# Optimization experiments

Measured on AMD Instinct MI355X. Metric: run time of the kernel, lower is better.

## Reference

```python
import jax, jax.numpy as jnp
from jax import lax
import numpy as np
import math

B, H, W = 2, 48, 48
D_MODEL, D_STATE, D_CONV, EXPAND = 96, 16, 3, 2
D_INNER = EXPAND * D_MODEL
DT_RANK = math.ceil(D_MODEL / 16)
K = 6
L = H * W


def setup_inputs():
    key = jax.random.key(0)
    ks = jax.random.split(key, 10)
    x = jax.random.normal(ks[0], (B, H, W, D_MODEL), jnp.float32)
    y = jax.random.normal(ks[1], (B, H, W, D_MODEL), jnp.float32)
    k = jax.random.normal(ks[2], (B, H, W, D_MODEL), jnp.float32)
    in_proj_w = jax.random.normal(ks[3], (2 * D_INNER, D_MODEL), jnp.float32) * 0.02
    conv_w = jax.random.normal(ks[4], (D_INNER, 1, D_CONV, D_CONV), jnp.float32) * 0.1
    conv_b = jnp.zeros((D_INNER,), jnp.float32)
    x_proj_w = jax.random.normal(ks[5], (K, DT_RANK + 2 * D_STATE, D_INNER), jnp.float32) * 0.02
    s = DT_RANK ** -0.5
    dt_w = jax.random.uniform(ks[6], (K, D_INNER, DT_RANK), jnp.float32, -s, s)
    dt = jnp.exp(jax.random.uniform(ks[7], (K, D_INNER), jnp.float32)
                 * (math.log(0.1) - math.log(0.001)) + math.log(0.001))
    dt_b = dt + jnp.log(-jnp.expm1(-dt))  # inverse-softplus init as in dt_init
    A_logs = jnp.tile(jnp.log(jnp.arange(1, D_STATE + 1, dtype=jnp.float32))[None],
                      (K * D_INNER, 1))
    Ds = jnp.ones((K * D_INNER,), jnp.float32)
    ln_w = jnp.ones((D_INNER,), jnp.float32)
    ln_b = jnp.zeros((D_INNER,), jnp.float32)
    out_proj_w = jax.random.normal(ks[8], (D_MODEL, D_INNER), jnp.float32) * 0.02
    return dict(x=x, y=y, k=k, in_proj_w=in_proj_w, conv_w=conv_w, conv_b=conv_b,
                x_proj_w=x_proj_w, dt_w=dt_w, dt_b=dt_b, A_logs=A_logs, Ds=Ds,
                ln_w=ln_w, ln_b=ln_b, out_proj_w=out_proj_w)


def _diag_gather(t):
    # out[b,c,h,w] = t[b,c,h,(h+w)%W]; then (H,W)->(W,H) transpose, flatten
    idx = (jnp.arange(H)[:, None] + jnp.arange(W)[None, :]) % W
    g = jnp.take_along_axis(t, idx[None, None], axis=3)
    return jnp.swapaxes(g, -1, -2).reshape(t.shape[0], t.shape[1], L)


def _diag_scatter(flat):
    # inverse of _diag_gather: result[b,c,h,w] = r[b,c,h,(w-h)%W]
    r = jnp.swapaxes(flat.reshape(flat.shape[0], flat.shape[1], W, H), -1, -2)
    inv = (jnp.arange(W)[None, :] - jnp.arange(H)[:, None]) % W
    return jnp.take_along_axis(r, inv[None, None], axis=3)


def _forward(x, y, k, in_proj_w, conv_w, conv_b, x_proj_w, dt_w, dt_b,
             A_logs, Ds, ln_w, ln_b, out_proj_w):
    xv = jnp.einsum('bhwc,oc->bhwo', x, in_proj_w)[..., :D_INNER]
    yv = jnp.einsum('bhwc,oc->bhwo', y, in_proj_w)[..., :D_INNER]
    # NOTE: torch code overwrites z three times; the surviving gate z comes from k
    z = jnp.einsum('bhwc,oc->bhwo', k, in_proj_w)[..., D_INNER:]

    def conv_act(t):
        t = jnp.transpose(t, (0, 3, 1, 2))  # NCHW
        t = lax.conv_general_dilated(t, conv_w, (1, 1), ((1, 1), (1, 1)),
                                     feature_group_count=D_INNER,
                                     dimension_numbers=('NCHW', 'OIHW', 'NCHW'))
        return jax.nn.silu(t + conv_b[None, :, None, None])

    xc = conv_act(xv)  # (B,d,H,W)
    yc = conv_act(yv)

    h_x = xc.reshape(B, D_INNER, L)                                   # row-major
    v_y = jnp.swapaxes(yc, 2, 3).reshape(B, D_INNER, L)               # column-major
    diag_z = _diag_gather(yc)                                         # diagonal
    highfreq = jnp.stack([h_x, v_y, diag_z], axis=1)                  # (B,3,d,L)
    xs = jnp.concatenate([highfreq, jnp.flip(highfreq, axis=-1)], axis=1)  # (B,K,d,L)

    x_dbl = jnp.einsum('bkdl,kcd->bkcl', xs, x_proj_w)
    dts = jnp.einsum('bkrl,kdr->bkdl', x_dbl[:, :, :DT_RANK], dt_w)
    Bs = x_dbl[:, :, DT_RANK:DT_RANK + D_STATE]                       # (B,K,N,L)
    Cs = x_dbl[:, :, DT_RANK + D_STATE:]                              # (B,K,N,L)

    delta = jax.nn.softplus(dts + dt_b[None, :, :, None])             # (B,K,d,L)
    A = -jnp.exp(A_logs).reshape(K, D_INNER, D_STATE)
    Dk = Ds.reshape(K, D_INNER)

    def step(h, inp):
        dl, ul, Bl, Cl = inp  # (B,K,d),(B,K,d),(B,K,N),(B,K,N)
        h = jnp.exp(dl[..., None] * A) * h + (dl * ul)[..., None] * Bl[:, :, None, :]
        return h, jnp.einsum('bkdn,bkn->bkd', h, Cl)

    h0 = jnp.zeros((B, K, D_INNER, D_STATE), jnp.float32)
    seq = (jnp.moveaxis(delta, -1, 0), jnp.moveaxis(xs, -1, 0),
           jnp.moveaxis(Bs, -1, 0), jnp.moveaxis(Cs, -1, 0))
    _, ys = lax.scan(step, h0, seq)
    out_y = jnp.moveaxis(ys, 0, -1) + Dk[None, :, :, None] * xs       # (B,K,d,L)

    inv_y = jnp.flip(out_y[:, 3:6], axis=-1)

    def unT(t):  # undo the (W,H) raster used by vertical direction
        return jnp.swapaxes(t.reshape(B, D_INNER, W, H), -1, -2).reshape(B, D_INNER, L)

    y_h = out_y[:, 0] + inv_y[:, 0]
    y_v = unT(out_y[:, 1]) + unT(inv_y[:, 1])
    y_D = (_diag_scatter(out_y[:, 2]) + _diag_scatter(inv_y[:, 2])).reshape(B, D_INNER, L)

    zg = jax.nn.silu(z)

    def head(t):
        t = jnp.swapaxes(t, 1, 2).reshape(B, H, W, D_INNER)
        mu = t.mean(-1, keepdims=True)
        var = ((t - mu) ** 2).mean(-1, keepdims=True)
        t = (t - mu) * lax.rsqrt(var + 1e-5) * ln_w + ln_b
        return jnp.einsum('bhwd,od->bhwo', t * zg, out_proj_w)

    return head(y_h), head(y_v), head(y_D)


def reference(x, y, k, in_proj_w, conv_w, conv_b, x_proj_w, dt_w, dt_b,
              A_logs, Ds, ln_w, ln_b, out_proj_w):
    return _forward(x, y, k, in_proj_w, conv_w, conv_b, x_proj_w, dt_w, dt_b,
                    A_logs, Ds, ln_w, ln_b, out_proj_w)
```

## Files before the change

### kernel.cpp

```cpp
#include <hip/hip_runtime.h>
#include <hip/hip_bf16.h>

namespace {

constexpr int B_ = 2, H_ = 48, W_ = 48, DM_ = 96, DI_ = 192, NS_ = 16, RK_ = 6, K_ = 6;
constexpr int L_ = H_ * W_;
constexpr int C_ = 144;
constexpr int LC_ = L_ / C_;
constexpr int NPROJ = RK_ + 2 * NS_;
constexpr int NPAD = 48;

__device__ __forceinline__ float sigmoidf_(float x) { return 1.f / (1.f + __expf(-x)); }

__device__ __forceinline__ float delta_of(const float* __restrict__ dp,
                                          const float* __restrict__ wdt,
                                          float bias) {
  float s = bias;
#pragma unroll
  for (int r = 0; r < RK_; ++r) s += dp[r] * wdt[r];
  return (s > 20.f) ? s : __logf(1.f + __expf(s));
}

__device__ __forceinline__ int src_row(int k, int pos) {
  int pk = (k >= 3) ? (L_ - 1 - pos) : pos;
  int kk = (k >= 3) ? k - 3 : k;
  if (kk == 0) return pk;
  int h = pk % H_, wcol = pk / H_;
  if (kk == 1) return h * W_ + wcol;
  return h * W_ + (wcol + h) % W_;
}

constexpr int IM = 32, IBK = 32;
__global__ void __launch_bounds__(256) k_inproj2(
    const float* __restrict__ x, const float* __restrict__ y,
    const float* __restrict__ kin, const float* __restrict__ inpw,
    float* __restrict__ xv, float* __restrict__ yv, float* __restrict__ zg) {
  __shared__ float As[IM][IBK + 1];
  __shared__ float Ws[IBK][DI_ + 1];
  int tid = threadIdx.x;
  constexpr int BPS = (B_ * L_) / IM;
  int s = blockIdx.x / BPS;
  int row0 = (blockIdx.x % BPS) * IM;
  const float* src = (s == 0) ? x : (s == 1) ? y : kin;
  float* dst = (s == 0) ? xv : (s == 1) ? yv : zg;
  int nbase = (s == 2) ? DI_ : 0;
  int tm = tid >> 4, tn = tid & 15;
  float acc[2][12];
#pragma unroll
  for (int i = 0; i < 2; ++i)
#pragma unroll
    for (int j = 0; j < 12; ++j) acc[i][j] = 0.f;

  for (int k0 = 0; k0 < DM_; k0 += IBK) {
    {
      int r = tid >> 3, c4 = (tid & 7) << 2;
      const float4 v = *reinterpret_cast<const float4*>(
          &src[(size_t)(row0 + r) * DM_ + k0 + c4]);
      As[r][c4] = v.x; As[r][c4 + 1] = v.y; As[r][c4 + 2] = v.z; As[r][c4 + 3] = v.w;
    }
#pragma unroll
    for (int it = 0; it < 6; ++it) {
      int i = tid + it * 256;
      int col = i >> 3, k4 = (i & 7) << 2;
      const float4 v = *reinterpret_cast<const float4*>(
          &inpw[(size_t)(nbase + col) * DM_ + k0 + k4]);
      Ws[k4 + 0][col] = v.x; Ws[k4 + 1][col] = v.y;
      Ws[k4 + 2][col] = v.z; Ws[k4 + 3][col] = v.w;
    }
    __syncthreads();
#pragma unroll
    for (int kk = 0; kk < IBK; ++kk) {
      float a0 = As[tm * 2 + 0][kk], a1 = As[tm * 2 + 1][kk];
      float w[12];
#pragma unroll
      for (int j = 0; j < 12; ++j) w[j] = Ws[kk][tn * 12 + j];
#pragma unroll
      for (int j = 0; j < 12; ++j) {
        acc[0][j] += a0 * w[j];
        acc[1][j] += a1 * w[j];
      }
    }
    __syncthreads();
  }
#pragma unroll
  for (int i = 0; i < 2; ++i) {
    size_t ob = (size_t)(row0 + tm * 2 + i) * DI_ + tn * 12;
#pragma unroll
    for (int j4 = 0; j4 < 3; ++j4) {
      float4 v;
      v.x = acc[i][j4 * 4 + 0]; v.y = acc[i][j4 * 4 + 1];
      v.z = acc[i][j4 * 4 + 2]; v.w = acc[i][j4 * 4 + 3];
      if (s == 2) {
        v.x *= sigmoidf_(v.x); v.y *= sigmoidf_(v.y);
        v.z *= sigmoidf_(v.z); v.w *= sigmoidf_(v.w);
      }
      *reinterpret_cast<float4*>(&dst[ob + j4 * 4]) = v;
    }
  }
}

__global__ void __launch_bounds__(192) k_conv2(
    const float* __restrict__ xv, const float* __restrict__ yv,
    const float* __restrict__ cw, const float* __restrict__ cb,
    float* __restrict__ xc, float* __restrict__ yc) {
  __shared__ float scw[9 * DI_];
  int tid = threadIdx.x;
  for (int i = tid; i < 9 * DI_; i += 192) {
    int d = i / 9, j = i % 9;
    scw[j * DI_ + d] = cw[i];
  }
  __syncthreads();
  int p = tid / 48, q = tid % 48;
  int gl = blockIdx.x * 4 + p;
  int b = gl / L_, l = gl % L_;
  int h = l / W_, w = l % W_;
  int d4 = q << 2;
  float4 ax = *reinterpret_cast<const float4*>(&cb[d4]);
  float4 ay = ax;
#pragma unroll
  for (int kh = 0; kh < 3; ++kh) {
    int hh = h + kh - 1;
    if ((unsigned)hh >= (unsigned)H_) continue;
#pragma unroll
    for (int kw = 0; kw < 3; ++kw) {
      int ww = w + kw - 1;
      if ((unsigned)ww >= (unsigned)W_) continue;
      float4 wk = *reinterpret_cast<const float4*>(&scw[(kh * 3 + kw) * DI_ + d4]);
      size_t idx = ((size_t)b * L_ + hh * W_ + ww) * DI_ + d4;
      float4 vx = *reinterpret_cast<const float4*>(&xv[idx]);
      float4 vy = *reinterpret_cast<const float4*>(&yv[idx]);
      ax.x += vx.x * wk.x; ax.y += vx.y * wk.y; ax.z += vx.z * wk.z; ax.w += vx.w * wk.w;
      ay.x += vy.x * wk.x; ay.y += vy.y * wk.y; ay.z += vy.z * wk.z; ay.w += vy.w * wk.w;
    }
  }
  ax.x *= sigmoidf_(ax.x); ax.y *= sigmoidf_(ax.y);
  ax.z *= sigmoidf_(ax.z); ax.w *= sigmoidf_(ax.w);
  ay.x *= sigmoidf_(ay.x); ay.y *= sigmoidf_(ay.y);
  ay.z *= sigmoidf_(ay.z); ay.w *= sigmoidf_(ay.w);
  size_t ob = (size_t)gl * DI_ + d4;
  *reinterpret_cast<float4*>(&xc[ob]) = ax;
  *reinterpret_cast<float4*>(&yc[ob]) = ay;
}

constexpr int XM = 32, XBK = 32;
__global__ void __launch_bounds__(256) k_xdbl3(
    const float* __restrict__ xc, const float* __restrict__ yc,
    const float* __restrict__ xpw,
    float* __restrict__ dts, float* __restrict__ Bsb, float* __restrict__ Csb) {
  __shared__ float As[XM][XBK + 1];
  __shared__ float Ws[XBK][NPAD];
  int tid = threadIdx.x;
  int row0 = blockIdx.x * XM;
  int b = row0 / (K_ * L_);
  int k = (row0 / L_) % K_;
  int pos0 = row0 % L_;
  const float* usrc = ((k == 0 || k == 3) ? xc : yc) + (size_t)b * L_ * DI_;
  int tm = tid >> 4, tn = tid & 15;
  for (int i = tid; i < XBK * (NPAD - NPROJ); i += 256) {
    int kk = i / (NPAD - NPROJ), c = NPROJ + i % (NPAD - NPROJ);
    Ws[kk][c] = 0.f;
  }
  float acc[2][3];
#pragma unroll
  for (int i = 0; i < 2; ++i)
#pragma unroll
    for (int j = 0; j < 3; ++j) acc[i][j] = 0.f;

  for (int k0 = 0; k0 < DI_; k0 += XBK) {
    {
      int r = tid >> 3, c4 = (tid & 7) << 2;
      int srow = src_row(k, pos0 + r);
      const float4 v = *reinterpret_cast<const float4*>(
          &usrc[(size_t)srow * DI_ + k0 + c4]);
      As[r][c4] = v.x; As[r][c4 + 1] = v.y; As[r][c4 + 2] = v.z; As[r][c4 + 3] = v.w;
    }
#pragma unroll
    for (int it = 0; it < 2; ++it) {
      int i = tid + it * 256;
      if (i < NPROJ * 8) {
        int c = i >> 3, k4 = (i & 7) << 2;
        const float4 v = *reinterpret_cast<const float4*>(
            &xpw[((size_t)k * NPROJ + c) * DI_ + k0 + k4]);
        Ws[k4 + 0][c] = v.x; Ws[k4 + 1][c] = v.y;
        Ws[k4 + 2][c] = v.z; Ws[k4 + 3][c] = v.w;
      }
    }
    __syncthreads();
#pragma unroll
    for (int kk = 0; kk < XBK; ++kk) {
      float a0 = As[tm * 2 + 0][kk], a1 = As[tm * 2 + 1][kk];
      float w0 = Ws[kk][tn * 3 + 0], w1 = Ws[kk][tn * 3 + 1], w2 = Ws[kk][tn * 3 + 2];
      acc[0][0] += a0 * w0; acc[0][1] += a0 * w1; acc[0][2] += a0 * w2;
      acc[1][0] += a1 * w0; acc[1][1] += a1 * w1; acc[1][2] += a1 * w2;
    }
    __syncthreads();
  }
#pragma unroll
  for (int i = 0; i < 2; ++i) {
    int row = row0 + tm * 2 + i;
#pragma unroll
    for (int j = 0; j < 3; ++j) {
      int cc = tn * 3 + j;
      float v = acc[i][j];
      if (cc < RK_) dts[(size_t)row * RK_ + cc] = v;
      else if (cc < RK_ + NS_) Bsb[(size_t)row * NS_ + (cc - RK_)] = v;
      else if (cc < NPROJ) Csb[(size_t)row * NS_ + (cc - RK_ - NS_)] = v;
    }
  }
}

__global__ void __launch_bounds__(192) k_scan1(
    const float* __restrict__ dts, const float* __restrict__ dtw,
    const float* __restrict__ dtb, const float* __restrict__ xc,
    const float* __restrict__ yc, const float* __restrict__ Bsb,
    const float* __restrict__ A_logs,
    float* __restrict__ Sdl, float* __restrict__ SHin) {
  __shared__ float sB[LC_ * NS_];
  __shared__ float sdt[LC_ * RK_];
  int blk = blockIdx.x;
  int bk = blk / C_, c = blk % C_;
  int b = bk / K_, k = bk % K_;
  int d = threadIdx.x;
  const float* usrc = ((k == 0 || k == 3) ? xc : yc) + (size_t)b * L_ * DI_;
  int pos0 = c * LC_;
  size_t base = (size_t)bk * L_ + pos0;
  for (int i = d; i < LC_ * NS_; i += 192) sB[i] = Bsb[base * NS_ + i];
  for (int i = d; i < LC_ * RK_; i += 192) sdt[i] = dts[base * RK_ + i];
  float A[NS_];
#pragma unroll
  for (int n = 0; n < NS_; ++n) A[n] = -__expf(A_logs[((size_t)k * DI_ + d) * NS_ + n]);
  float wdt[RK_];
#pragma unroll
  for (int r = 0; r < RK_; ++r) wdt[r] = dtw[((size_t)k * DI_ + d) * RK_ + r];
  float bias = dtb[k * DI_ + d];
  float S[NS_];
#pragma unroll
  for (int n = 0; n < NS_; ++n) S[n] = 0.f;
  float sum_dl = 0.f;
  __syncthreads();
  for (int l = 0; l < LC_; ++l) {
    float dl = delta_of(&sdt[l * RK_], wdt, bias);
    float u = usrc[(size_t)src_row(k, pos0 + l) * DI_ + d];
    float du = dl * u;
    sum_dl += dl;
    const float* Bp = &sB[l * NS_];
#pragma unroll
    for (int n = 0; n < NS_; ++n) {
      float e = __expf(dl * A[n]);
      S[n] = e * S[n] + du * Bp[n];
    }
  }
  Sdl[(size_t)blk * DI_ + d] = sum_dl;
  size_t ob = (size_t)blk * NS_ * DI_ + d;
#pragma unroll
  for (int n = 0; n < NS_; ++n) SHin[ob + (size_t)n * DI_] = S[n];
}

__global__ void __launch_bounds__(192) k_scan2(
    const float* __restrict__ Sdl, const float* __restrict__ A_logs,
    float* __restrict__ SHin) {
  int bkn = blockIdx.x;
  int bk = bkn / NS_, n = bkn % NS_;
  int k = bk % K_;
  int d = threadIdx.x;
  float A = -__expf(A_logs[((size_t)k * DI_ + d) * NS_ + n]);
  float h = 0.f;
  for (int c = 0; c < C_; ++c) {
    size_t i = ((size_t)(bk * C_ + c) * NS_ + n) * DI_ + d;
    float s = SHin[i];
    float p = __expf(A * Sdl[(size_t)(bk * C_ + c) * DI_ + d]);
    SHin[i] = h;
    h = p * h + s;
  }
}

__global__ void __launch_bounds__(192) k_scan3(
    const float* __restrict__ dts, const float* __restrict__ dtw,
    const float* __restrict__ dtb, const float* __restrict__ xc,
    const float* __restrict__ yc, const float* __restrict__ Bsb,
    const float* __restrict__ Csb, const float* __restrict__ A_logs,
    const float* __restrict__ Ds, const float* __restrict__ SHin,
    float* __restrict__ out_y) {
  __shared__ float sB[LC_ * NS_];
  __shared__ float sC[LC_ * NS_];
  __shared__ float sdt[LC_ * RK_];
  int blk = blockIdx.x;
  int bk = blk / C_, c = blk % C_;
  int b = bk / K_, k = bk % K_;
  int d = threadIdx.x;
  const float* usrc = ((k == 0 || k == 3) ? xc : yc) + (size_t)b * L_ * DI_;
  int pos0 = c * LC_;
  size_t base = (size_t)bk * L_ + pos0;
  for (int i = d; i < LC_ * NS_; i += 192) {
    sB[i] = Bsb[base * NS_ + i];
    sC[i] = Csb[base * NS_ + i];
  }
  for (int i = d; i < LC_ * RK_; i += 192) sdt[i] = dts[base * RK_ + i];
  float A[NS_];
#pragma unroll
  for (int n = 0; n < NS_; ++n) A[n] = -__expf(A_logs[((size_t)k * DI_ + d) * NS_ + n]);
  float wdt[RK_];
#pragma unroll
  for (int r = 0; r < RK_; ++r) wdt[r] = dtw[((size_t)k * DI_ + d) * RK_ + r];
  float bias = dtb[k * DI_ + d];
  float Dk = Ds[k * DI_ + d];
  float h[NS_];
  size_t hb = (size_t)blk * NS_ * DI_ + d;
#pragma unroll
  for (int n = 0; n < NS_; ++n) h[n] = SHin[hb + (size_t)n * DI_];
  __syncthreads();
  for (int l = 0; l < LC_; ++l) {
    float dl = delta_of(&sdt[l * RK_], wdt, bias);
    float u = usrc[(size_t)src_row(k, pos0 + l) * DI_ + d];
    float du = dl * u;
    const float* Bp = &sB[l * NS_];
    const float* Cp = &sC[l * NS_];
    float yacc = 0.f;
#pragma unroll
    for (int n = 0; n < NS_; ++n) {
      h[n] = __expf(dl * A[n]) * h[n] + du * Bp[n];
      yacc += h[n] * Cp[n];
    }
    out_y[(base + l) * DI_ + d] = yacc + Dk * u;
  }
}

constexpr int MT = 32, GS_ = 196;
__global__ void __launch_bounds__(256) k_head2(
    const float* __restrict__ out_y, const float* __restrict__ zg,
    const float* __restrict__ lnw, const float* __restrict__ lnb,
    const float* __restrict__ opw, float* __restrict__ out) {
  __shared__ float Gs[MT][GS_];
  __shared__ float Ws[32][DM_ + 1];
  int tid = threadIdx.x;
  constexpr int BPS = (B_ * L_) / MT;
  int m = blockIdx.x / BPS;
  int r0 = (blockIdx.x % BPS) * MT;

  {
    int row = tid >> 3, t8 = tid & 7;
    int bl = r0 + row;
    int b = bl / L_, lp = bl % L_;
    int h = lp / W_, w = lp % W_;
    int l0;
    if (m == 0) l0 = lp;
    else if (m == 1) l0 = w * H_ + h;
    else l0 = ((w - h + W_) % W_) * H_ + h;
    size_t basef = ((size_t)b * K_ + m) * L_;
    size_t baser = ((size_t)b * K_ + m + 3) * L_;
    const float* pf = out_y + (basef + l0) * DI_;
    const float* pr = out_y + (baser + (size_t)(L_ - 1 - l0)) * DI_;
    float s = 0.f, s2 = 0.f;
#pragma unroll
    for (int j = 0; j < 6; ++j) {
      int c4 = t8 * 24 + j * 4;
      float4 a = *reinterpret_cast<const float4*>(&pf[c4]);
      float4 bb = *reinterpret_cast<const float4*>(&pr[c4]);
      float4 t;
      t.x = a.x + bb.x; t.y = a.y + bb.y; t.z = a.z + bb.z; t.w = a.w + bb.w;
      s += t.x + t.y + t.z + t.w;
      s2 += t.x * t.x + t.y * t.y + t.z * t.z + t.w * t.w;
      *reinterpret_cast<float4*>(&Gs[row][c4]) = t;
    }
    s += __shfl_xor(s, 1, 64);  s2 += __shfl_xor(s2, 1, 64);
    s += __shfl_xor(s, 2, 64);  s2 += __shfl_xor(s2, 2, 64);
    s += __shfl_xor(s, 4, 64);  s2 += __shfl_xor(s2, 4, 64);
    float mu = s * (1.f / DI_);
    float var = fmaxf(s2 * (1.f / DI_) - mu * mu, 0.f);
    float rs = rsqrtf(var + 1e-5f);
    const float* zp = zg + (size_t)bl * DI_;
#pragma unroll
    for (int j = 0; j < 6; ++j) {
      int c4 = t8 * 24 + j * 4;
      float4 t = *reinterpret_cast<const float4*>(&Gs[row][c4]);
      float4 zv = *reinterpret_cast<const float4*>(&zp[c4]);
      t.x = ((t.x - mu) * rs * lnw[c4 + 0] + lnb[c4 + 0]) * zv.x;
      t.y = ((t.y - mu) * rs * lnw[c4 + 1] + lnb[c4 + 1]) * zv.y;
      t.z = ((t.z - mu) * rs * lnw[c4 + 2] + lnb[c4 + 2]) * zv.z;
      t.w = ((t.w - mu) * rs * lnw[c4 + 3] + lnb[c4 + 3]) * zv.w;
      *reinterpret_cast<float4*>(&Gs[row][c4]) = t;
    }
  }
  __syncthreads();

  int tm = tid >> 4, tn = tid & 15;
  float acc[2][6];
#pragma unroll
  for (int i = 0; i < 2; ++i)
#pragma unroll
    for (int j = 0; j < 6; ++j) acc[i][j] = 0.f;

  for (int k0 = 0; k0 < DI_; k0 += 32) {
#pragma unroll
    for (int it = 0; it < 3; ++it) {
      int i = tid + it * 256;
      int o = i >> 3, k4 = (i & 7) << 2;
      const float4 v = *reinterpret_cast<const float4*>(
          &opw[(size_t)o * DI_ + k0 + k4]);
      Ws[k4 + 0][o] = v.x; Ws[k4 + 1][o] = v.y;
      Ws[k4 + 2][o] = v.z; Ws[k4 + 3][o] = v.w;
    }
    __syncthreads();
#pragma unroll
    for (int kk = 0; kk < 32; ++kk) {
      float a0 = Gs[tm * 2 + 0][k0 + kk], a1 = Gs[tm * 2 + 1][k0 + kk];
      float w[6];
#pragma unroll
      for (int j = 0; j < 6; ++j) w[j] = Ws[kk][tn * 6 + j];
#pragma unroll
      for (int j = 0; j < 6; ++j) {
        acc[0][j] += a0 * w[j];
        acc[1][j] += a1 * w[j];
      }
    }
    __syncthreads();
  }
  size_t obase = ((size_t)m * (B_ * L_) + r0) * DM_;
#pragma unroll
  for (int i = 0; i < 2; ++i) {
    size_t ob = obase + (size_t)(tm * 2 + i) * DM_ + tn * 6;
#pragma unroll
    for (int j = 0; j < 6; ++j) out[ob + j] = acc[i][j];
  }
}

}

extern "C" void kernel_launch(void* const* d_in, const int* in_sizes, int n_in,
                              void* d_out, int out_size, void* d_ws, size_t ws_size,
                              hipStream_t stream) {
  const float* x = (const float*)d_in[0];
  const float* y = (const float*)d_in[1];
  const float* kin = (const float*)d_in[2];
  const float* in_proj_w = (const float*)d_in[3];
  const float* conv_w = (const float*)d_in[4];
  const float* conv_b = (const float*)d_in[5];
  const float* x_proj_w = (const float*)d_in[6];
  const float* dt_w = (const float*)d_in[7];
  const float* dt_b = (const float*)d_in[8];
  const float* A_logs = (const float*)d_in[9];
  const float* Ds = (const float*)d_in[10];
  const float* ln_w = (const float*)d_in[11];
  const float* ln_b = (const float*)d_in[12];
  const float* out_proj_w = (const float*)d_in[13];
  float* out = (float*)d_out;

  float* ws = (float*)d_ws;
  const size_t BLD = (size_t)B_ * L_ * DI_;
  const size_t BKLD = (size_t)B_ * K_ * L_ * DI_;
  const size_t BKLN = (size_t)B_ * K_ * L_ * NS_;
  const size_t PSN = (size_t)B_ * K_ * C_ * NS_ * DI_;
  float* xv = ws;     ws += BLD;
  float* yv = ws;     ws += BLD;
  float* zg = ws;     ws += BLD;
  float* xc = ws;     ws += BLD;
  float* yc = ws;     ws += BLD;
  float* Bsb = ws;    ws += BKLN;
  float* Csb = ws;    ws += BKLN;
  float* out_y = ws;  ws += BKLD;
  float* SHin = ws;   ws += PSN;
  float* Sdl = ws;    ws += (size_t)B_ * K_ * C_ * DI_;
  float* dts = ws;    ws += (size_t)B_ * K_ * L_ * RK_;

  k_inproj2<<<3 * B_ * L_ / IM, 256, 0, stream>>>(x, y, kin, in_proj_w, xv, yv, zg);
  k_conv2<<<B_ * L_ / 4, 192, 0, stream>>>(xv, yv, conv_w, conv_b, xc, yc);
  k_xdbl3<<<B_ * K_ * L_ / XM, 256, 0, stream>>>(xc, yc, x_proj_w, dts, Bsb, Csb);
  k_scan1<<<B_ * K_ * C_, 192, 0, stream>>>(dts, dt_w, dt_b, xc, yc, Bsb, A_logs,
                                            Sdl, SHin);
  k_scan2<<<B_ * K_ * NS_, 192, 0, stream>>>(Sdl, A_logs, SHin);
  k_scan3<<<B_ * K_ * C_, 192, 0, stream>>>(dts, dt_w, dt_b, xc, yc, Bsb, Csb,
                                            A_logs, Ds, SHin, out_y);
  k_head2<<<3 * B_ * L_ / MT, 256, 0, stream>>>(out_y, zg, ln_w, ln_b, out_proj_w, out);
}
```

Measured before the change: 161.3 us.

## Fuse x_proj GEMM with chunked scan pass one into single kernel

Merges the x_proj projection kernel and the first chunk-scan kernel. Each block now stages a full 32-row by 192-channel activation tile in shared memory and keeps the projected dt/B/C rows in shared memory. It then runs the local scan for two 16-length chunks directly, avoiding a kernel launch and the re-reads of dts, Bsb and the activations from global memory. The trade-off is much larger shared memory per block, which may lower occupancy, and only 192 of 256 threads take part in the serial scan phase.

```diff
diff --git a/kernel.cpp b/kernel.cpp
--- a/kernel.cpp
+++ b/kernel.cpp
@@ -142,13 +142,16 @@
   *reinterpret_cast<float4*>(&yc[ob]) = ay;
 }
 
-constexpr int XM = 32, XBK = 32;
-__global__ void __launch_bounds__(256) k_xdbl3(
+constexpr int XM = 32, XBK = 32, XAS = 196;
+__global__ void __launch_bounds__(256) k_xdbl_scan1(
     const float* __restrict__ xc, const float* __restrict__ yc,
-    const float* __restrict__ xpw,
-    float* __restrict__ dts, float* __restrict__ Bsb, float* __restrict__ Csb) {
-  __shared__ float As[XM][XBK + 1];
+    const float* __restrict__ xpw, const float* __restrict__ dtw,
+    const float* __restrict__ dtb, const float* __restrict__ A_logs,
+    float* __restrict__ dts, float* __restrict__ Bsb, float* __restrict__ Csb,
+    float* __restrict__ Sdl, float* __restrict__ SHin) {
+  __shared__ float As[XM][XAS];
   __shared__ float Ws[XBK][NPAD];
+  __shared__ float xd[XM][NPAD + 1];
   int tid = threadIdx.x;
   int row0 = blockIdx.x * XM;
   int b = row0 / (K_ * L_);
@@ -156,6 +159,16 @@
   int pos0 = row0 % L_;
   const float* usrc = ((k == 0 || k == 3) ? xc : yc) + (size_t)b * L_ * DI_;
   int tm = tid >> 4, tn = tid & 15;
+
+#pragma unroll
+  for (int it = 0; it < 6; ++it) {
+    int i = tid + it * 256;
+    int r = i / 48, c4 = (i % 48) << 2;
+    int srow = src_row(k, pos0 + r);
+    const float4 v = *reinterpret_cast<const float4*>(
+        &usrc[(size_t)srow * DI_ + c4]);
+    As[r][c4] = v.x; As[r][c4 + 1] = v.y; As[r][c4 + 2] = v.z; As[r][c4 + 3] = v.w;
+  }
   for (int i = tid; i < XBK * (NPAD - NPROJ); i += 256) {
     int kk = i / (NPAD - NPROJ), c = NPROJ + i % (NPAD - NPROJ);
     Ws[kk][c] = 0.f;
@@ -167,13 +180,6 @@
     for (int j = 0; j < 3; ++j) acc[i][j] = 0.f;
 
   for (int k0 = 0; k0 < DI_; k0 += XBK) {
-    {
-      int r = tid >> 3, c4 = (tid & 7) << 2;
-      int srow = src_row(k, pos0 + r);
-      const float4 v = *reinterpret_cast<const float4*>(
-          &usrc[(size_t)srow * DI_ + k0 + c4]);
-      As[r][c4] = v.x; As[r][c4 + 1] = v.y; As[r][c4 + 2] = v.z; As[r][c4 + 3] = v.w;
-    }
 #pragma unroll
     for (int it = 0; it < 2; ++it) {
       int i = tid + it * 256;
@@ -188,7 +194,7 @@
     __syncthreads();
 #pragma unroll
     for (int kk = 0; kk < XBK; ++kk) {
-      float a0 = As[tm * 2 + 0][kk], a1 = As[tm * 2 + 1][kk];
+      float a0 = As[tm * 2 + 0][k0 + kk], a1 = As[tm * 2 + 1][k0 + kk];
       float w0 = Ws[kk][tn * 3 + 0], w1 = Ws[kk][tn * 3 + 1], w2 = Ws[kk][tn * 3 + 2];
       acc[0][0] += a0 * w0; acc[0][1] += a0 * w1; acc[0][2] += a0 * w2;
       acc[1][0] += a1 * w0; acc[1][1] += a1 * w1; acc[1][2] += a1 * w2;
@@ -197,63 +203,56 @@
   }
 #pragma unroll
   for (int i = 0; i < 2; ++i) {
-    int row = row0 + tm * 2 + i;
+    int r = tm * 2 + i;
+    int row = row0 + r;
 #pragma unroll
     for (int j = 0; j < 3; ++j) {
       int cc = tn * 3 + j;
       float v = acc[i][j];
+      xd[r][cc] = v;
       if (cc < RK_) dts[(size_t)row * RK_ + cc] = v;
       else if (cc < RK_ + NS_) Bsb[(size_t)row * NS_ + (cc - RK_)] = v;
       else if (cc < NPROJ) Csb[(size_t)row * NS_ + (cc - RK_ - NS_)] = v;
     }
   }
-}
-
-__global__ void __launch_bounds__(192) k_scan1(
-    const float* __restrict__ dts, const float* __restrict__ dtw,
-    const float* __restrict__ dtb, const float* __restrict__ xc,
-    const float* __restrict__ yc, const float* __restrict__ Bsb,
-    const float* __restrict__ A_logs,
-    float* __restrict__ Sdl, float* __restrict__ SHin) {
-  __shared__ float sB[LC_ * NS_];
-  __shared__ float sdt[LC_ * RK_];
-  int blk = blockIdx.x;
-  int bk = blk / C_, c = blk % C_;
-  int b = bk / K_, k = bk % K_;
-  int d = threadIdx.x;
-  const float* usrc = ((k == 0 || k == 3) ? xc : yc) + (size_t)b * L_ * DI_;
-  int pos0 = c * LC_;
-  size_t base = (size_t)bk * L_ + pos0;
-  for (int i = d; i < LC_ * NS_; i += 192) sB[i] = Bsb[base * NS_ + i];
-  for (int i = d; i < LC_ * RK_; i += 192) sdt[i] = dts[base * RK_ + i];
-  float A[NS_];
-#pragma unroll
-  for (int n = 0; n < NS_; ++n) A[n] = -__expf(A_logs[((size_t)k * DI_ + d) * NS_ + n]);
-  float wdt[RK_];
-#pragma unroll
-  for (int r = 0; r < RK_; ++r) wdt[r] = dtw[((size_t)k * DI_ + d) * RK_ + r];
-  float bias = dtb[k * DI_ + d];
-  float S[NS_];
-#pragma unroll
-  for (int n = 0; n < NS_; ++n) S[n] = 0.f;
-  float sum_dl = 0.f;
   __syncthreads();
-  for (int l = 0; l < LC_; ++l) {
-    float dl = delta_of(&sdt[l * RK_], wdt, bias);
-    float u = usrc[(size_t)src_row(k, pos0 + l) * DI_ + d];
-    float du = dl * u;
-    sum_dl += dl;
-    const float* Bp = &sB[l * NS_];
-#pragma unroll
-    for (int n = 0; n < NS_; ++n) {
-      float e = __expf(dl * A[n]);
-      S[n] = e * S[n] + du * Bp[n];
-    }
-  }
-  Sdl[(size_t)blk * DI_ + d] = sum_dl;
-  size_t ob = (size_t)blk * NS_ * DI_ + d;
-#pragma unroll
-  for (int n = 0; n < NS_; ++n) SHin[ob + (size_t)n * DI_] = S[n];
+
+  if (tid < DI_) {
+    int d = tid;
+    float A[NS_];
+#pragma unroll
+    for (int n = 0; n < NS_; ++n)
+      A[n] = -__expf(A_logs[((size_t)k * DI_ + d) * NS_ + n]);
+    float wdt[RK_];
+#pragma unroll
+    for (int r = 0; r < RK_; ++r) wdt[r] = dtw[((size_t)k * DI_ + d) * RK_ + r];
+    float bias = dtb[k * DI_ + d];
+#pragma unroll
+    for (int ch = 0; ch < 2; ++ch) {
+      float S[NS_];
+#pragma unroll
+      for (int n = 0; n < NS_; ++n) S[n] = 0.f;
+      float sum_dl = 0.f;
+      for (int l = 0; l < LC_; ++l) {
+        int r = ch * LC_ + l;
+        float dl = delta_of(&xd[r][0], wdt, bias);
+        float u = As[r][d];
+        float du = dl * u;
+        sum_dl += dl;
+        const float* Bp = &xd[r][RK_];
+#pragma unroll
+        for (int n = 0; n < NS_; ++n) {
+          float e = __expf(dl * A[n]);
+          S[n] = e * S[n] + du * Bp[n];
+        }
+      }
+      int gchunk = blockIdx.x * 2 + ch;
+      Sdl[(size_t)gchunk * DI_ + d] = sum_dl;
+      size_t ob = (size_t)gchunk * NS_ * DI_ + d;
+#pragma unroll
+      for (int n = 0; n < NS_; ++n) SHin[ob + (size_t)n * DI_] = S[n];
+    }
+  }
 }
 
 __global__ void __launch_bounds__(192) k_scan2(
@@ -464,9 +463,8 @@
 
   k_inproj2<<<3 * B_ * L_ / IM, 256, 0, stream>>>(x, y, kin, in_proj_w, xv, yv, zg);
   k_conv2<<<B_ * L_ / 4, 192, 0, stream>>>(xv, yv, conv_w, conv_b, xc, yc);
-  k_xdbl3<<<B_ * K_ * L_ / XM, 256, 0, stream>>>(xc, yc, x_proj_w, dts, Bsb, Csb);
-  k_scan1<<<B_ * K_ * C_, 192, 0, stream>>>(dts, dt_w, dt_b, xc, yc, Bsb, A_logs,
-                                            Sdl, SHin);
+  k_xdbl_scan1<<<B_ * K_ * L_ / XM, 256, 0, stream>>>(xc, yc, x_proj_w, dt_w, dt_b,
+                                                      A_logs, dts, Bsb, Csb, Sdl, SHin);
   k_scan2<<<B_ * K_ * NS_, 192, 0, stream>>>(Sdl, A_logs, SHin);
   k_scan3<<<B_ * K_ * C_, 192, 0, stream>>>(dts, dt_w, dt_b, xc, yc, Bsb, Csb,
                                             A_logs, Ds, SHin, out_y);
```

Result: no change. 159.2 us (-1.3%).
